# Performance work log

Hardware: AMD Instinct MI355X
Metric: run time of the kernel (lower is better)

## Reference

```python
import jax, jax.numpy as jnp
import numpy as np

N_NODES = 50000
N_EDGES = 1600000
IN_FEAT = 128
HIDDEN = 128
CLASSES = 2


def gin_conv(x, src, dst, W, b, n_nodes):
    # GINConv (eps=0): h_i = mlp(x_i + sum_{j in N(i)} x_j)
    agg = jax.ops.segment_sum(x[src], dst, num_segments=n_nodes)  # [N, F]
    h = x + agg
    return h @ W + b


def setup_inputs() -> dict:
    key = jax.random.key(0)
    ks = jax.random.split(key, 8)
    x = jax.random.normal(ks[0], (N_NODES, IN_FEAT), dtype=jnp.float32)
    edge_index = jax.random.randint(ks[1], (2, N_EDGES), 0, N_NODES, dtype=jnp.int64)
    def lin(k, fan_in, fan_out):
        kw, kb = jax.random.split(k)
        bound = 1.0 / np.sqrt(fan_in)
        W = jax.random.uniform(kw, (fan_in, fan_out), jnp.float32, -bound, bound)
        b = jax.random.uniform(kb, (fan_out,), jnp.float32, -bound, bound)
        return W, b
    W1, b1 = lin(ks[2], IN_FEAT, HIDDEN)
    W2, b2 = lin(ks[3], HIDDEN, HIDDEN)
    W3, b3 = lin(ks[4], HIDDEN, CLASSES)
    return {"x": x, "edge_index": edge_index, "W1": W1, "b1": b1,
            "W2": W2, "b2": b2, "W3": W3, "b3": b3}


def reference(x, edge_index, W1, b1, W2, b2, W3, b3):
    src, dst = edge_index[0], edge_index[1]
    n = x.shape[0]
    h = jax.nn.relu(gin_conv(x, src, dst, W1, b1, n))
    h = jax.nn.relu(gin_conv(h, src, dst, W2, b2, n))
    return gin_conv(h, src, dst, W3, b3, n)
```

## Files before the change

kernel.cpp:

```cpp
#include <hip/hip_runtime.h>

#define NNODES 50000
#define NEDGES 1600000
#define F 128

#define NB 256
#define BSH 196
#define BCAP 6784
#define EPT 10

typedef __attribute__((ext_vector_type(8))) short bf16x8;
typedef __attribute__((ext_vector_type(4))) float f32x4;

__device__ inline unsigned short f2bf(float f) {
    union { float f; unsigned u; } v; v.f = f;
    unsigned r = v.u + 0x7FFF + ((v.u >> 16) & 1);
    return (unsigned short)(r >> 16);
}
__device__ inline float2 up2(ushort2 h) {
    union { unsigned u; float f; } a, b;
    a.u = ((unsigned)h.x) << 16; b.u = ((unsigned)h.y) << 16;
    return make_float2(a.f, b.f);
}
__device__ inline float b2f(unsigned short h) {
    union { unsigned u; float f; } a;
    a.u = ((unsigned)h) << 16;
    return a.f;
}

__global__ __launch_bounds__(256) void cvt_bf16(const float4* __restrict__ in,
                                                ushort4* __restrict__ out, int n4) {
    int i = blockIdx.x * blockDim.x + threadIdx.x;
    int stride = gridDim.x * blockDim.x;
    for (; i < n4; i += stride) {
        float4 v = in[i];
        ushort4 o;
        o.x = f2bf(v.x); o.y = f2bf(v.y); o.z = f2bf(v.z); o.w = f2bf(v.w);
        out[i] = o;
    }
}

__global__ __launch_bounds__(256) void wprep2(const float* __restrict__ W1,
                                              const float* __restrict__ W2,
                                              unsigned short* __restrict__ Wf1,
                                              unsigned short* __restrict__ Wf2,
                                              int* __restrict__ gcnt) {
    int id = blockIdx.x * 256 + threadIdx.x;
    if (blockIdx.x == 0) gcnt[threadIdx.x] = 0;
    const float* W = (id < 2048) ? W1 : W2;
    unsigned short* Wf = (id < 2048) ? Wf1 : Wf2;
    id &= 2047;
    const int l = id & 63, nn = (id >> 6) & 7, s = id >> 9;
    const int c = nn * 16 + (l & 15);
    const int k0 = s * 32 + (l >> 4) * 8;
    ushort4 lo, hi;
    lo.x = f2bf(W[(k0 + 0) * F + c]); lo.y = f2bf(W[(k0 + 1) * F + c]);
    lo.z = f2bf(W[(k0 + 2) * F + c]); lo.w = f2bf(W[(k0 + 3) * F + c]);
    hi.x = f2bf(W[(k0 + 4) * F + c]); hi.y = f2bf(W[(k0 + 5) * F + c]);
    hi.z = f2bf(W[(k0 + 6) * F + c]); hi.w = f2bf(W[(k0 + 7) * F + c]);
    ushort4* p = (ushort4*)(Wf + (size_t)id * 8);
    p[0] = lo; p[1] = hi;
}

__global__ __launch_bounds__(256) void bucketA(const int* __restrict__ src,
                                               const int* __restrict__ dst,
                                               unsigned* __restrict__ E1,
                                               int* __restrict__ gcnt) {
    __shared__ unsigned hist[4][NB];
    __shared__ unsigned start[4][NB];
    const int t = threadIdx.x, w = t >> 6;
    for (int i = t; i < 4 * NB; i += 256) ((unsigned*)hist)[i] = 0;
    __syncthreads();
    const int base = blockIdx.x * (256 * EPT);
    unsigned rec[EPT]; int bkt[EPT]; unsigned rnk[EPT];
#pragma unroll
    for (int k = 0; k < EPT; ++k) {
        const int i = base + k * 256 + t;
        const int s = src[i], d = dst[i];
        const int b = d / BSH;
        rec[k] = ((unsigned)s << 8) | (unsigned)(d - b * BSH);
        bkt[k] = b;
        rnk[k] = atomicAdd(&hist[w][b], 1u);
    }
    __syncthreads();
    {
        const unsigned h0 = hist[0][t], h1 = hist[1][t], h2 = hist[2][t], h3 = hist[3][t];
        const unsigned tot = h0 + h1 + h2 + h3;
        const unsigned g = tot ? (unsigned)atomicAdd(&gcnt[t], (int)tot) : 0u;
        start[0][t] = g;
        start[1][t] = g + h0;
        start[2][t] = g + h0 + h1;
        start[3][t] = g + h0 + h1 + h2;
    }
    __syncthreads();
#pragma unroll
    for (int k = 0; k < EPT; ++k) {
        const unsigned p = start[w][bkt[k]] + rnk[k];
        if (p < BCAP) E1[(size_t)bkt[k] * BCAP + p] = rec[k];
    }
}

__global__ __launch_bounds__(256) void bucketB(const unsigned* __restrict__ E1,
                                               const int* __restrict__ gcnt,
                                               int* __restrict__ off,
                                               unsigned short* __restrict__ ssrc) {
    __shared__ int cnt[BSH];
    __shared__ int cur[BSH];
    __shared__ int wtot[4];
    __shared__ int bst[NB];
    const int b = blockIdx.x, t = threadIdx.x;
    if (t < 64) {
        const int a0 = gcnt[t * 4], a1 = gcnt[t * 4 + 1];
        const int a2 = gcnt[t * 4 + 2], a3 = gcnt[t * 4 + 3];
        const int s = a0 + a1 + a2 + a3;
        int inc = s;
#pragma unroll
        for (int o = 1; o <= 32; o <<= 1) {
            int u = __shfl_up(inc, o);
            if (t >= o) inc += u;
        }
        const int e = inc - s;
        bst[t * 4] = e;
        bst[t * 4 + 1] = e + a0;
        bst[t * 4 + 2] = e + a0 + a1;
        bst[t * 4 + 3] = e + a0 + a1 + a2;
    }
    for (int i = t; i < BSH; i += 256) cnt[i] = 0;
    __syncthreads();
    const int ne = min(gcnt[b], BCAP);
    const int ebase = bst[b];
    const unsigned* E = E1 + (size_t)b * BCAP;
    for (int i = t; i < ne; i += 256) atomicAdd(&cnt[E[i] & 255], 1);
    __syncthreads();
    const int val = (t < BSH) ? cnt[t] : 0;
    int inc = val;
    const int lane = t & 63, w = t >> 6;
#pragma unroll
    for (int o = 1; o <= 32; o <<= 1) {
        int u = __shfl_up(inc, o);
        if (lane >= o) inc += u;
    }
    if (lane == 63) wtot[w] = inc;
    __syncthreads();
    int woff = 0;
    for (int k = 0; k < w; ++k) woff += wtot[k];
    const int excl = woff + inc - val;
    if (t < BSH) {
        cur[t] = excl;
        const int n = b * BSH + t;
        if (n < NNODES) off[n] = ebase + excl;
    }
    if (b == NB - 1 && t == 0) off[NNODES] = NEDGES;
    __syncthreads();
    for (int i = t; i < ne; i += 256) {
        const unsigned rec = E[i];
        const int r = atomicAdd(&cur[rec & 255], 1);
        ssrc[ebase + r] = (unsigned short)(rec >> 8);
    }
}

__global__ __launch_bounds__(64) void agg_bf16(const ushort2* __restrict__ h,
                                               const int* __restrict__ off,
                                               const unsigned short* __restrict__ ssrc,
                                               ushort2* __restrict__ S, int n) {
    const int wid = blockIdx.x;
    const int lane = threadIdx.x;
    const int e0 = off[wid], e1 = off[wid + 1];
    float2 acc = up2(h[(size_t)wid * 64 + lane]);
    for (int base = e0; base < e1; base += 64) {
        const int cnt = min(64, e1 - base);
        const int myidx = (base + lane < e1) ? (int)ssrc[base + lane] : 0;
        int i = 0;
        for (; i + 16 <= cnt; i += 16) {
            float2 v[16];
#pragma unroll
            for (int k = 0; k < 16; ++k) {
                const int s = __shfl(myidx, i + k);
                v[k] = up2(h[(size_t)s * 64 + lane]);
            }
            float x0 = 0.f, y0 = 0.f;
#pragma unroll
            for (int k = 0; k < 16; ++k) { x0 += v[k].x; y0 += v[k].y; }
            acc.x += x0; acc.y += y0;
        }
        for (; i + 4 <= cnt; i += 4) {
            const int s0 = __shfl(myidx, i + 0), s1 = __shfl(myidx, i + 1);
            const int s2 = __shfl(myidx, i + 2), s3 = __shfl(myidx, i + 3);
            const float2 v0 = up2(h[(size_t)s0 * 64 + lane]);
            const float2 v1 = up2(h[(size_t)s1 * 64 + lane]);
            const float2 v2 = up2(h[(size_t)s2 * 64 + lane]);
            const float2 v3 = up2(h[(size_t)s3 * 64 + lane]);
            acc.x += (v0.x + v1.x) + (v2.x + v3.x);
            acc.y += (v0.y + v1.y) + (v2.y + v3.y);
        }
        for (; i < cnt; ++i) {
            const int s = __shfl(myidx, i);
            const float2 v = up2(h[(size_t)s * 64 + lane]);
            acc.x += v.x;
            acc.y += v.y;
        }
    }
    ushort2 o;
    o.x = f2bf(acc.x); o.y = f2bf(acc.y);
    S[(size_t)wid * 64 + lane] = o;
}

__global__ __launch_bounds__(256) void mlp_mfma(const unsigned short* __restrict__ Sb,
                                                const unsigned short* __restrict__ Wfrag,
                                                const float* __restrict__ bias,
                                                unsigned short* __restrict__ Hb,
                                                int n, int relu) {
    const int wave = threadIdx.x >> 6, lane = threadIdx.x & 63;
    const int base = blockIdx.x * 64 + wave * 16;
    const int r16 = lane & 15, hi = lane >> 4;
    int arow = base + r16;
    if (arow >= n) arow = n - 1;
    const unsigned short* Arow = Sb + (size_t)arow * F;

    f32x4 acc[8];
#pragma unroll
    for (int i = 0; i < 8; ++i) acc[i] = (f32x4){0.f, 0.f, 0.f, 0.f};

#pragma unroll
    for (int s = 0; s < 4; ++s) {
        const bf16x8 a = *(const bf16x8*)(Arow + s * 32 + hi * 8);
#pragma unroll
        for (int nn = 0; nn < 8; ++nn) {
            const bf16x8 b = *(const bf16x8*)(Wfrag + ((size_t)(s * 8 + nn) * 64 + lane) * 8);
            acc[nn] = __builtin_amdgcn_mfma_f32_16x16x32_bf16(a, b, acc[nn], 0, 0, 0);
        }
    }

#pragma unroll
    for (int nn = 0; nn < 8; ++nn) {
        const int col = nn * 16 + r16;
        const float bv = bias[col];
#pragma unroll
        for (int r = 0; r < 4; ++r) {
            const int row = base + hi * 4 + r;
            if (row < n) {
                float v = acc[nn][r] + bv;
                if (relu) v = fmaxf(v, 0.f);
                Hb[(size_t)row * F + col] = f2bf(v);
            }
        }
    }
}

__global__ __launch_bounds__(256) void head_t(const unsigned short* __restrict__ Hb,
                                              const float4* __restrict__ W3,
                                              float2* __restrict__ y, int n) {
    const int wid = (blockIdx.x * blockDim.x + threadIdx.x) >> 6;
    const int lane = threadIdx.x & 63;
    if (wid >= n) return;
    const unsigned short* hp = Hb + (size_t)wid * F + lane * 2;
    const float hx = b2f(hp[0]), hy = b2f(hp[1]);
    const float4 w = W3[lane];
    float a0 = hx * w.x + hy * w.z;
    float a1 = hx * w.y + hy * w.w;
#pragma unroll
    for (int o = 32; o; o >>= 1) {
        a0 += __shfl_xor(a0, o);
        a1 += __shfl_xor(a1, o);
    }
    if (lane == 0) y[wid] = make_float2(a0, a1);
}

__global__ __launch_bounds__(256) void agg3(const float2* __restrict__ y,
                                            const int* __restrict__ off,
                                            const unsigned short* __restrict__ ssrc,
                                            const float* __restrict__ b3,
                                            float2* __restrict__ out, int n) {
    const int i = blockIdx.x * blockDim.x + threadIdx.x;
    if (i >= n) return;
    float2 acc = y[i];
    const int e1 = off[i + 1];
    for (int e = off[i]; e < e1; ++e) {
        const float2 v = y[ssrc[e]];
        acc.x += v.x;
        acc.y += v.y;
    }
    out[i] = make_float2(acc.x + b3[0], acc.y + b3[1]);
}

extern "C" void kernel_launch(void* const* d_in, const int* in_sizes, int n_in,
                              void* d_out, int out_size, void* d_ws, size_t ws_size,
                              hipStream_t stream) {
    const float* x  = (const float*)d_in[0];
    const int* ei   = (const int*)d_in[1];
    const int* src  = ei;
    const int* dst  = ei + NEDGES;
    const float* W1 = (const float*)d_in[2];
    const float* b1 = (const float*)d_in[3];
    const float* W2 = (const float*)d_in[4];
    const float* b2 = (const float*)d_in[5];
    const float* W3 = (const float*)d_in[6];
    const float* b3 = (const float*)d_in[7];
    float* out = (float*)d_out;

    char* ws = (char*)d_ws;
    const size_t featB = (size_t)NNODES * F * 2;
    unsigned short* xb = (unsigned short*)ws;
    unsigned short* Sb = (unsigned short*)(ws + featB);
    unsigned short* Hb = (unsigned short*)(ws + 2 * featB);
    char* p = ws + 3 * featB;
    float* y3 = (float*)p;                 p += (size_t)NNODES * 2 * 4 + 256;
    unsigned short* Wf1 = (unsigned short*)p; p += 2048 * 8 * 2;
    unsigned short* Wf2 = (unsigned short*)p; p += 2048 * 8 * 2;
    unsigned* E1 = (unsigned*)p;           p += (size_t)NB * BCAP * 4;
    int* gcnt = (int*)p;                   p += NB * 4 + 256;
    int* off = (int*)p;                    p += (size_t)(NNODES + 1) * 4 + 256;
    unsigned short* ssrc = (unsigned short*)p;

    cvt_bf16<<<1024, 256, 0, stream>>>((const float4*)x, (ushort4*)xb, NNODES * F / 4);
    wprep2<<<16, 256, 0, stream>>>(W1, W2, Wf1, Wf2, gcnt);

    bucketA<<<NEDGES / (256 * EPT), 256, 0, stream>>>(src, dst, E1, gcnt);
    bucketB<<<NB, 256, 0, stream>>>(E1, gcnt, off, ssrc);

    const int mlpBlocks = (NNODES + 63) / 64;

    agg_bf16<<<NNODES, 64, 0, stream>>>((const ushort2*)xb, off, ssrc, (ushort2*)Sb, NNODES);
    mlp_mfma<<<mlpBlocks, 256, 0, stream>>>(Sb, Wf1, b1, Hb, NNODES, 1);

    agg_bf16<<<NNODES, 64, 0, stream>>>((const ushort2*)Hb, off, ssrc, (ushort2*)Sb, NNODES);
    mlp_mfma<<<mlpBlocks, 256, 0, stream>>>(Sb, Wf2, b2, xb, NNODES, 1);

    head_t<<<(NNODES + 3) / 4, 256, 0, stream>>>(xb, (const float4*)W3, (float2*)y3, NNODES);
    agg3<<<(NNODES + 255) / 256, 256, 0, stream>>>((const float2*)y3, off, ssrc, b3, (float2*)out, NNODES);
}
```

Before: 276.3 us.

## Merge bf16 convert, weight prep and edge bucketing into one prep kernel

Fuses the x-to-bf16 conversion, weight swizzle and the first bucketing pass into a single launch partitioned by block index, with the counter reset moved to a memset. It also doubles the bucket count and halves bucket width so the second pass sorts smaller segments with more blocks. Packed record bits shrink from 8 to 7 for the local destination, which still fits 98 nodes and leaves room for a 16-bit source index. The aim is fewer launches and better parallelism in bucketB, at the cost of a tighter per-bucket capacity margin (3500 slots against an expected ~3136).

```diff
diff --git a/kernel.cpp b/kernel.cpp
--- a/kernel.cpp
+++ b/kernel.cpp
@@ -4,10 +4,14 @@
 #define NEDGES 1600000
 #define F 128
 
-#define NB 256
-#define BSH 196
-#define BCAP 6784
+#define NB 512
+#define BSH 98
+#define BCAP 3500
 #define EPT 10
+
+#define PREP_A 625
+#define PREP_CVT 512
+#define PREP_W 16
 
 typedef __attribute__((ext_vector_type(8))) short bf16x8;
 typedef __attribute__((ext_vector_type(4))) float f32x4;
@@ -28,75 +32,78 @@
     return a.f;
 }
 
-__global__ __launch_bounds__(256) void cvt_bf16(const float4* __restrict__ in,
-                                                ushort4* __restrict__ out, int n4) {
-    int i = blockIdx.x * blockDim.x + threadIdx.x;
-    int stride = gridDim.x * blockDim.x;
-    for (; i < n4; i += stride) {
-        float4 v = in[i];
-        ushort4 o;
-        o.x = f2bf(v.x); o.y = f2bf(v.y); o.z = f2bf(v.z); o.w = f2bf(v.w);
-        out[i] = o;
-    }
-}
-
-__global__ __launch_bounds__(256) void wprep2(const float* __restrict__ W1,
-                                              const float* __restrict__ W2,
-                                              unsigned short* __restrict__ Wf1,
-                                              unsigned short* __restrict__ Wf2,
-                                              int* __restrict__ gcnt) {
-    int id = blockIdx.x * 256 + threadIdx.x;
-    if (blockIdx.x == 0) gcnt[threadIdx.x] = 0;
-    const float* W = (id < 2048) ? W1 : W2;
-    unsigned short* Wf = (id < 2048) ? Wf1 : Wf2;
-    id &= 2047;
-    const int l = id & 63, nn = (id >> 6) & 7, s = id >> 9;
-    const int c = nn * 16 + (l & 15);
-    const int k0 = s * 32 + (l >> 4) * 8;
-    ushort4 lo, hi;
-    lo.x = f2bf(W[(k0 + 0) * F + c]); lo.y = f2bf(W[(k0 + 1) * F + c]);
-    lo.z = f2bf(W[(k0 + 2) * F + c]); lo.w = f2bf(W[(k0 + 3) * F + c]);
-    hi.x = f2bf(W[(k0 + 4) * F + c]); hi.y = f2bf(W[(k0 + 5) * F + c]);
-    hi.z = f2bf(W[(k0 + 6) * F + c]); hi.w = f2bf(W[(k0 + 7) * F + c]);
-    ushort4* p = (ushort4*)(Wf + (size_t)id * 8);
-    p[0] = lo; p[1] = hi;
-}
-
-__global__ __launch_bounds__(256) void bucketA(const int* __restrict__ src,
-                                               const int* __restrict__ dst,
-                                               unsigned* __restrict__ E1,
-                                               int* __restrict__ gcnt) {
-    __shared__ unsigned hist[4][NB];
-    __shared__ unsigned start[4][NB];
-    const int t = threadIdx.x, w = t >> 6;
-    for (int i = t; i < 4 * NB; i += 256) ((unsigned*)hist)[i] = 0;
-    __syncthreads();
-    const int base = blockIdx.x * (256 * EPT);
-    unsigned rec[EPT]; int bkt[EPT]; unsigned rnk[EPT];
-#pragma unroll
-    for (int k = 0; k < EPT; ++k) {
-        const int i = base + k * 256 + t;
-        const int s = src[i], d = dst[i];
-        const int b = d / BSH;
-        rec[k] = ((unsigned)s << 8) | (unsigned)(d - b * BSH);
-        bkt[k] = b;
-        rnk[k] = atomicAdd(&hist[w][b], 1u);
-    }
-    __syncthreads();
-    {
-        const unsigned h0 = hist[0][t], h1 = hist[1][t], h2 = hist[2][t], h3 = hist[3][t];
-        const unsigned tot = h0 + h1 + h2 + h3;
-        const unsigned g = tot ? (unsigned)atomicAdd(&gcnt[t], (int)tot) : 0u;
-        start[0][t] = g;
-        start[1][t] = g + h0;
-        start[2][t] = g + h0 + h1;
-        start[3][t] = g + h0 + h1 + h2;
-    }
-    __syncthreads();
-#pragma unroll
-    for (int k = 0; k < EPT; ++k) {
-        const unsigned p = start[w][bkt[k]] + rnk[k];
-        if (p < BCAP) E1[(size_t)bkt[k] * BCAP + p] = rec[k];
+__global__ __launch_bounds__(256) void prep(const float* __restrict__ x,
+                                            const int* __restrict__ src,
+                                            const int* __restrict__ dst,
+                                            const float* __restrict__ W1,
+                                            const float* __restrict__ W2,
+                                            unsigned short* __restrict__ xb,
+                                            unsigned short* __restrict__ Wf1,
+                                            unsigned short* __restrict__ Wf2,
+                                            unsigned* __restrict__ E1,
+                                            int* __restrict__ gcnt) {
+    const int bid = blockIdx.x;
+    const int t = threadIdx.x;
+    if (bid < PREP_A) {
+        __shared__ unsigned hist[4][NB];
+        __shared__ unsigned start[4][NB];
+        const int w = t >> 6;
+        for (int i = t; i < 4 * NB; i += 256) ((unsigned*)hist)[i] = 0;
+        __syncthreads();
+        const int base = bid * (256 * EPT);
+        unsigned rec[EPT]; int bkt[EPT]; unsigned rnk[EPT];
+#pragma unroll
+        for (int k = 0; k < EPT; ++k) {
+            const int i = base + k * 256 + t;
+            const int s = src[i], d = dst[i];
+            const int b = d / BSH;
+            rec[k] = ((unsigned)s << 7) | (unsigned)(d - b * BSH);
+            bkt[k] = b;
+            rnk[k] = atomicAdd(&hist[w][b], 1u);
+        }
+        __syncthreads();
+        for (int b = t; b < NB; b += 256) {
+            const unsigned h0 = hist[0][b], h1 = hist[1][b], h2 = hist[2][b], h3 = hist[3][b];
+            const unsigned tot = h0 + h1 + h2 + h3;
+            const unsigned g = tot ? (unsigned)atomicAdd(&gcnt[b], (int)tot) : 0u;
+            start[0][b] = g;
+            start[1][b] = g + h0;
+            start[2][b] = g + h0 + h1;
+            start[3][b] = g + h0 + h1 + h2;
+        }
+        __syncthreads();
+#pragma unroll
+        for (int k = 0; k < EPT; ++k) {
+            const unsigned p = start[w][bkt[k]] + rnk[k];
+            if (p < BCAP) E1[(size_t)bkt[k] * BCAP + p] = rec[k];
+        }
+    } else if (bid < PREP_A + PREP_CVT) {
+        const int n4 = NNODES * F / 4;
+        const float4* in = (const float4*)x;
+        ushort4* out = (ushort4*)xb;
+        int i = (bid - PREP_A) * 256 + t;
+        const int stride = PREP_CVT * 256;
+        for (; i < n4; i += stride) {
+            float4 v = in[i];
+            ushort4 o;
+            o.x = f2bf(v.x); o.y = f2bf(v.y); o.z = f2bf(v.z); o.w = f2bf(v.w);
+            out[i] = o;
+        }
+    } else {
+        int id = (bid - PREP_A - PREP_CVT) * 256 + t;
+        const float* W = (id < 2048) ? W1 : W2;
+        unsigned short* Wf = (id < 2048) ? Wf1 : Wf2;
+        id &= 2047;
+        const int l = id & 63, nn = (id >> 6) & 7, s = id >> 9;
+        const int c = nn * 16 + (l & 15);
+        const int k0 = s * 32 + (l >> 4) * 8;
+        ushort4 lo, hi;
+        lo.x = f2bf(W[(k0 + 0) * F + c]); lo.y = f2bf(W[(k0 + 1) * F + c]);
+        lo.z = f2bf(W[(k0 + 2) * F + c]); lo.w = f2bf(W[(k0 + 3) * F + c]);
+        hi.x = f2bf(W[(k0 + 4) * F + c]); hi.y = f2bf(W[(k0 + 5) * F + c]);
+        hi.z = f2bf(W[(k0 + 6) * F + c]); hi.w = f2bf(W[(k0 + 7) * F + c]);
+        ushort4* p = (ushort4*)(Wf + (size_t)id * 8);
+        p[0] = lo; p[1] = hi;
     }
 }
 
@@ -110,27 +117,25 @@
     __shared__ int bst[NB];
     const int b = blockIdx.x, t = threadIdx.x;
     if (t < 64) {
-        const int a0 = gcnt[t * 4], a1 = gcnt[t * 4 + 1];
-        const int a2 = gcnt[t * 4 + 2], a3 = gcnt[t * 4 + 3];
-        const int s = a0 + a1 + a2 + a3;
+        int a[8]; int s = 0;
+#pragma unroll
+        for (int k = 0; k < 8; ++k) { a[k] = gcnt[t * 8 + k]; s += a[k]; }
         int inc = s;
 #pragma unroll
         for (int o = 1; o <= 32; o <<= 1) {
             int u = __shfl_up(inc, o);
             if (t >= o) inc += u;
         }
-        const int e = inc - s;
-        bst[t * 4] = e;
-        bst[t * 4 + 1] = e + a0;
-        bst[t * 4 + 2] = e + a0 + a1;
-        bst[t * 4 + 3] = e + a0 + a1 + a2;
+        int e = inc - s;
+#pragma unroll
+        for (int k = 0; k < 8; ++k) { bst[t * 8 + k] = e; e += a[k]; }
     }
     for (int i = t; i < BSH; i += 256) cnt[i] = 0;
     __syncthreads();
     const int ne = min(gcnt[b], BCAP);
     const int ebase = bst[b];
     const unsigned* E = E1 + (size_t)b * BCAP;
-    for (int i = t; i < ne; i += 256) atomicAdd(&cnt[E[i] & 255], 1);
+    for (int i = t; i < ne; i += 256) atomicAdd(&cnt[E[i] & 127], 1);
     __syncthreads();
     const int val = (t < BSH) ? cnt[t] : 0;
     int inc = val;
@@ -154,8 +159,8 @@
     __syncthreads();
     for (int i = t; i < ne; i += 256) {
         const unsigned rec = E[i];
-        const int r = atomicAdd(&cur[rec & 255], 1);
-        ssrc[ebase + r] = (unsigned short)(rec >> 8);
+        const int r = atomicAdd(&cur[rec & 127], 1);
+        ssrc[ebase + r] = (unsigned short)(rec >> 7);
     }
 }
 
@@ -312,10 +317,9 @@
     int* off = (int*)p;                    p += (size_t)(NNODES + 1) * 4 + 256;
     unsigned short* ssrc = (unsigned short*)p;
 
-    cvt_bf16<<<1024, 256, 0, stream>>>((const float4*)x, (ushort4*)xb, NNODES * F / 4);
-    wprep2<<<16, 256, 0, stream>>>(W1, W2, Wf1, Wf2, gcnt);
-
-    bucketA<<<NEDGES / (256 * EPT), 256, 0, stream>>>(src, dst, E1, gcnt);
+    hipMemsetAsync(gcnt, 0, NB * sizeof(int), stream);
+    prep<<<PREP_A + PREP_CVT + PREP_W, 256, 0, stream>>>(x, src, dst, W1, W2,
+                                                         xb, Wf1, Wf2, E1, gcnt);
     bucketB<<<NB, 256, 0, stream>>>(E1, gcnt, off, ssrc);
 
     const int mlpBlocks = (NNODES + 63) / 64;
```

Result: faster. 267.5 us (-3.2%).
